# Optimization experiments

Measured on AMD Instinct MI355X. Metric: run time of the kernel, lower is better.

## Reference

```python
import jax, jax.numpy as jnp
import numpy as np
import math

NUM_HEADS = 16
HEAVY_RATIO = 0.1
RECENT_RATIO = 0.1
ROPE_THETA = 10000.0


def setup_inputs() -> dict:
    key = jax.random.key(0)
    ks = jax.random.split(key, 5)
    b, s, h = 1, 2048, 2048
    return {
        "hidden_states": jax.random.normal(ks[0], (b, s, h), dtype=jnp.float32),
        "Wq": jax.random.normal(ks[1], (h, h), dtype=jnp.float32) * 0.02,
        "Wk": jax.random.normal(ks[2], (h, h), dtype=jnp.float32) * 0.02,
        "Wv": jax.random.normal(ks[3], (h, h), dtype=jnp.float32) * 0.02,
        "Wo": jax.random.normal(ks[4], (h, h), dtype=jnp.float32) * 0.02,
    }


def _rotate_half(x):
    d = x.shape[-1]
    return jnp.concatenate([-x[..., d // 2:], x[..., : d // 2]], axis=-1)


def _rope(q, k, seq_len, head_dim, dtype):
    # LLaMA rotary embedding: inv_freq over even dims, emb = [freqs, freqs]
    inv_freq = 1.0 / (ROPE_THETA ** (jnp.arange(0, head_dim, 2, dtype=jnp.float32) / head_dim))
    pos = jnp.arange(seq_len, dtype=jnp.float32)
    freqs = pos[:, None] * inv_freq[None, :]            # [s, d/2]
    emb = jnp.concatenate([freqs, freqs], axis=-1)       # [s, d]
    cos = jnp.cos(emb).astype(dtype)[None, None]         # [1,1,s,d]
    sin = jnp.sin(emb).astype(dtype)[None, None]
    q = q * cos + _rotate_half(q) * sin
    k = k * cos + _rotate_half(k) * sin
    return q, k


def reference(hidden_states, Wq, Wk, Wv, Wo):
    b, s, hidden = hidden_states.shape
    H = NUM_HEADS
    d = hidden // H

    def proj(W):  # nn.Linear(x) = x @ W.T, then split heads -> [b,H,s,d]
        return (hidden_states @ W.T).reshape(b, s, H, d).transpose(0, 2, 1, 3)

    q, k, v = proj(Wq), proj(Wk), proj(Wv)
    q, k = _rope(q, k, s, d, hidden_states.dtype)

    scores = jnp.einsum("bhqd,bhkd->bhqk", q, k) / math.sqrt(d)  # [b,H,s,s]
    neg = jnp.finfo(scores.dtype).min
    i = jnp.arange(s)[:, None]
    j = jnp.arange(s)[None, :]
    causal = jnp.where(j <= i, jnp.array(0.0, scores.dtype), neg)
    scores = jnp.maximum(scores + causal, neg)

    heavy_budget = int(HEAVY_RATIO * s)
    recent_budget = int(RECENT_RATIO * s)

    # first softmax (fp32), accumulate column importances
    tmp_attn = jax.nn.softmax(scores.astype(jnp.float32), axis=-1).astype(scores.dtype)
    tmp_sum = jnp.sum(tmp_attn, axis=-2)                 # [b,H,s]
    _, topk_idx = jax.lax.top_k(tmp_sum, heavy_budget)   # [b,H,heavy]
    heavy_mask = jnp.any(topk_idx[..., :, None] == jnp.arange(s)[None, None, None, :], axis=-2)  # [b,H,s]

    # recent band: tril(diag=recent) & triu(diag=-recent)  <=>  |i-j| <= recent
    band = jnp.abs(i - j) <= recent_budget               # [s,s]
    mask = heavy_mask[:, :, None, :] | band[None, None]

    scores = jnp.where(mask, scores, neg)
    probs = jax.nn.softmax(scores.astype(jnp.float32), axis=-1).astype(q.dtype)
    attn = jnp.einsum("bhqk,bhkd->bhqd", probs, v)
    attn = attn.transpose(0, 2, 1, 3).reshape(b, s, hidden)
    return attn @ Wo.T
```

## Files before the change

kernel.cpp:

```cpp
#include <hip/hip_runtime.h>
#include <hip/hip_bf16.h>
#include <stdint.h>

#define SEQ   2048
#define HIDN  2048
#define NHEAD 16
#define HDIM  128
#define HEAVY 204
#define RECENT 204

typedef __attribute__((ext_vector_type(4))) float f32x4;
typedef __attribute__((ext_vector_type(8))) short bf16x8;
typedef unsigned short u16;
typedef unsigned int   u32;

static __device__ __forceinline__ u16 f2bf(float f){
  union { float f; u32 u; } v; v.f = f;
  u32 r = (v.u + 0x7FFFu + ((v.u >> 16) & 1u)) >> 16;
  return (u16)r;
}
static __device__ __forceinline__ float bf2f(u16 u){
  union { u32 u; float f; } v; v.u = ((u32)u) << 16;
  return v.f;
}

static __device__ __forceinline__ void gload16(const void* g, void* l){
  __builtin_amdgcn_global_load_lds((const __attribute__((address_space(1))) u32*)g,
                                   (__attribute__((address_space(3))) u32*)l, 16, 0, 0);
}

#define WAITVM(N) asm volatile("s_waitcnt vmcnt(" #N ")" ::: "memory")
#define BARRAW    __builtin_amdgcn_s_barrier()
#define PRIO1     __builtin_amdgcn_s_setprio(1)
#define PRIO0     __builtin_amdgcn_s_setprio(0)

static __device__ __forceinline__ void stage_tile(const u16* __restrict__ base, size_t stride,
                                                  int row0, u16* __restrict__ lds, int tid){
  const int wbase = tid & ~63;
#pragma unroll
  for (int it = 0; it < 4; ++it){
    int m = it * 256 + tid;
    int row = m >> 4, cp = m & 15;
    gload16(base + (size_t)(row0 + row) * stride + ((cp ^ (row & 7)) * 8),
            lds + (it * 256 + wbase) * 8);
  }
}

static __device__ __forceinline__ void stageK512(const u16* __restrict__ base, size_t stride,
                                                 int row0, u16* __restrict__ lds, int tid){
#pragma unroll
  for (int it = 0; it < 2; ++it){
    int m = it * 512 + tid;
    int row = m >> 4, cp = m & 15;
    gload16(base + (size_t)(row0 + row) * stride + ((cp ^ (row & 7)) * 8),
            lds + (it * 512 + (tid & ~63)) * 8);
  }
}
static __device__ __forceinline__ void stageV512(const u16* __restrict__ base, size_t stride,
                                                 int c0, u16* __restrict__ lds, int tid){
#pragma unroll
  for (int it = 0; it < 2; ++it){
    int m = it * 512 + tid;
    int row = m >> 3, cp = m & 7;
    gload16(base + (size_t)row * stride + c0 + ((cp ^ (row & 7)) * 8),
            lds + (it * 512 + (tid & ~63)) * 8);
  }
}

__global__ void k_prep(const float* __restrict__ A0, const float* __restrict__ A1,
                       const float* __restrict__ A2, const float* __restrict__ A3,
                       const float* __restrict__ A4, u16* __restrict__ out,
                       float* __restrict__ cosT, float* __restrict__ sinT,
                       float* __restrict__ colsum){
  int b = blockIdx.x, tid = threadIdx.x;
  if (b < 20480){
    int id = b * 256 + tid;
    int sel = id >> 20, off = (id & 1048575) * 4;
    const float* src = sel == 0 ? A0 : sel == 1 ? A1 : sel == 2 ? A2 : sel == 3 ? A3 : A4;
    float4 v = *(const float4*)(src + off);
    ushort4 o;
    o.x = f2bf(v.x); o.y = f2bf(v.y); o.z = f2bf(v.z); o.w = f2bf(v.w);
    *(ushort4*)(out + (size_t)sel * 4194304 + off) = o;
  } else if (b < 20992){
    int i = (b - 20480) * 256 + tid;
    int pos = i >> 6, j = i & 63;
    float invf = powf(10000.0f, -(float)j * (1.0f / 64.0f));
    float a = (float)pos * invf;
    cosT[i] = cosf(a);
    sinT[i] = sinf(a);
  } else {
    int i = (b - 20992) * 256 + tid;
    if (i < 16384) ((float4*)colsum)[i] = (float4){0.f, 0.f, 0.f, 0.f};
  }
}

__global__ void k_post(u16* __restrict__ Qm, u16* __restrict__ Km,
                       const float* __restrict__ cosT, const float* __restrict__ sinT,
                       const u16* __restrict__ V, u16* __restrict__ Vt){
  __shared__ u16 t[32][33];
  int b = blockIdx.x, tid = threadIdx.x;
  if (b < 4096){
    int gid = b * 256 + tid;
    u16* M = (gid < 524288) ? Qm : Km;
    int id = gid & 524287;
    int pos = id >> 8, rem = id & 255;
    int h = rem >> 4, j4 = (rem & 15) * 4;
    u16* p = M + (size_t)pos * HIDN + h * HDIM + j4;
    ushort4 lo = *(ushort4*)p;
    ushort4 hi = *(ushort4*)(p + 64);
    float4 c = *(const float4*)(cosT + pos * 64 + j4);
    float4 s = *(const float4*)(sinT + pos * 64 + j4);
    float l0 = bf2f(lo.x), l1 = bf2f(lo.y), l2 = bf2f(lo.z), l3 = bf2f(lo.w);
    float h0 = bf2f(hi.x), h1 = bf2f(hi.y), h2 = bf2f(hi.z), h3 = bf2f(hi.w);
    ushort4 nlo, nhi;
    nlo.x = f2bf(l0 * c.x - h0 * s.x);  nhi.x = f2bf(h0 * c.x + l0 * s.x);
    nlo.y = f2bf(l1 * c.y - h1 * s.y);  nhi.y = f2bf(h1 * c.y + l1 * s.y);
    nlo.z = f2bf(l2 * c.z - h2 * s.z);  nhi.z = f2bf(h2 * c.z + l2 * s.z);
    nlo.w = f2bf(l3 * c.w - h3 * s.w);  nhi.w = f2bf(h3 * c.w + l3 * s.w);
    *(ushort4*)p = nlo;
    *(ushort4*)(p + 64) = nhi;
  } else {
    int b2 = b - 4096;
    int s0 = (b2 & 63) * 32, c0 = (b2 >> 6) * 32;
    int r = tid >> 3, cc = (tid & 7) * 4;
    ushort4 v = *(const ushort4*)(V + (size_t)(s0 + r) * 2048 + c0 + cc);
    t[r][cc] = v.x; t[r][cc + 1] = v.y; t[r][cc + 2] = v.z; t[r][cc + 3] = v.w;
    __syncthreads();
    int co = tid >> 3, ro = (tid & 7) * 4;
    ushort4 o;
    o.x = t[ro][co]; o.y = t[ro + 1][co]; o.z = t[ro + 2][co]; o.w = t[ro + 3][co];
    *(ushort4*)(Vt + (size_t)(c0 + co) * 2048 + s0 + ro) = o;
  }
}

__global__ __launch_bounds__(512, 1)
void k_g256(const u16* __restrict__ X, const u16* __restrict__ Wq, const u16* __restrict__ Wk,
            const u16* __restrict__ Wv, u16* __restrict__ C0, u16* __restrict__ C1,
            u16* __restrict__ C2){
  __shared__ __align__(16) u16 LA[2][256 * 64];
  __shared__ __align__(16) u16 LB[2][192 * 64];
  const int tid = threadIdx.x;
  const int lane = tid & 63, wvi = tid >> 6;
  const int wm = wvi >> 2, wn = wvi & 3;
  const int g = lane >> 4, c15 = lane & 15;
  const int brow = blockIdx.y * 256;
  const int bcol = blockIdx.x * 192;
  const int NT = 32;

  f32x4 acc[8][3];
#pragma unroll
  for (int m = 0; m < 8; m++)
#pragma unroll
    for (int n = 0; n < 3; n++) acc[m][n] = (f32x4){0.f, 0.f, 0.f, 0.f};

  const int cc0 = ((g ^ (c15 & 7)) * 8);
  bf16x8 af[4][2], bf[3][2];

#define BPTR(rB_) (rB_ < 2048 ? Wq + (size_t)(rB_) * 2048 \
                 : rB_ < 4096 ? Wk + (size_t)((rB_) - 2048) * 2048 \
                              : Wv + (size_t)((rB_) - 4096) * 2048)
#define STGA(grow0, gcol0, ldsb) do { \
  _Pragma("unroll") for (int it = 0; it < 2; ++it){ \
    int m_ = it * 512 + tid; \
    int row_ = m_ >> 3, cp_ = m_ & 7; \
    gload16(X + (size_t)((grow0) + row_) * 2048 + (gcol0) + ((cp_ ^ (row_ & 7)) * 8), \
            (ldsb) + (it * 512 + (tid & ~63)) * 8); \
  } } while(0)
#define STGB128(gcol0, ldsb) do { \
  _Pragma("unroll") for (int it = 0; it < 2; ++it){ \
    int m_ = it * 512 + tid; \
    int row_ = m_ >> 3, cp_ = m_ & 7; \
    int rB_ = bcol + row_; \
    const u16* bp_ = BPTR(rB_); \
    gload16(bp_ + (gcol0) + ((cp_ ^ (row_ & 7)) * 8), \
            (ldsb) + (it * 512 + (tid & ~63)) * 8); \
  } } while(0)
#define STGB64(gcol0, ldsb) do { \
    int row_ = 128 + (tid >> 3), cp_ = tid & 7; \
    int rB_ = bcol + row_; \
    const u16* bp_ = BPTR(rB_); \
    gload16(bp_ + (gcol0) + ((cp_ ^ (row_ & 7)) * 8), \
            (ldsb) + (tid & ~63) * 8); \
  } while(0)
#define RDA(buf, mibase) \
  _Pragma("unroll") for (int mi2 = 0; mi2 < 4; ++mi2){ \
    const u16* pr = &LA[buf][0] + (size_t)(wm * 128 + ((mibase) + mi2) * 16 + c15) * 64; \
    af[mi2][0] = *(const bf16x8*)(pr + cc0); \
    af[mi2][1] = *(const bf16x8*)(pr + (cc0 ^ 32)); \
  }
#define RDB2(buf) \
  _Pragma("unroll") for (int ni2 = 0; ni2 < 2; ++ni2){ \
    const u16* pr = &LB[buf][0] + (size_t)(wn * 48 + ni2 * 16 + c15) * 64; \
    bf[ni2][0] = *(const bf16x8*)(pr + cc0); \
    bf[ni2][1] = *(const bf16x8*)(pr + (cc0 ^ 32)); \
  }
#define RDB1(buf) do { \
    const u16* pr = &LB[buf][0] + (size_t)(wn * 48 + 32 + c15) * 64; \
    bf[2][0] = *(const bf16x8*)(pr + cc0); \
    bf[2][1] = *(const bf16x8*)(pr + (cc0 ^ 32)); \
  } while(0)
#define MM2(mibase) \
  _Pragma("unroll") for (int mi2 = 0; mi2 < 4; ++mi2) \
  _Pragma("unroll") for (int ni2 = 0; ni2 < 2; ++ni2) \
  _Pragma("unroll") for (int kk = 0; kk < 2; ++kk) \
    acc[(mibase) + mi2][ni2] = __builtin_amdgcn_mfma_f32_16x16x32_bf16( \
        af[mi2][kk], bf[ni2][kk], acc[(mibase) + mi2][ni2], 0, 0, 0);
#define MM1(mibase) \
  _Pragma("unroll") for (int mi2 = 0; mi2 < 4; ++mi2) \
  _Pragma("unroll") for (int kk = 0; kk < 2; ++kk) \
    acc[(mibase) + mi2][2] = __builtin_amdgcn_mfma_f32_16x16x32_bf16( \
        af[mi2][kk], bf[2][kk], acc[(mibase) + mi2][2], 0, 0, 0);

  STGA(brow,       0, &LA[0][0]);
  STGA(brow + 128, 0, &LA[0][0] + 128 * 64);
  STGB128(0,  &LB[0][0]);
  STGB64(0,   &LB[0][0] + 128 * 64);
  STGB128(64, &LB[1][0]);
  STGB64(64,  &LB[1][0] + 128 * 64);
  WAITVM(3);
  BARRAW;

  for (int t = 0; t < NT; t += 2){
    const int kn1 = (t + 1) * 64;
    const int kn2 = (t + 2) * 64;
    const int kn3 = (t + 3) * 64;
    RDA(0, 0); RDB2(0);
    STGA(brow, kn1, &LA[1][0]);
    BARRAW; PRIO1; MM2(0); PRIO0; BARRAW;
    RDB1(0);
    STGA(brow + 128, kn1, &LA[1][0] + 128 * 64);
    BARRAW; PRIO1; MM1(0); PRIO0; BARRAW;
    RDA(0, 4);
    if (t + 2 < NT) STGB128(kn2, &LB[0][0]);
    BARRAW; PRIO1; MM1(4); PRIO0; BARRAW;
    if (t + 2 < NT){ STGB64(kn2, &LB[0][0] + 128 * 64); WAITVM(3); }
    else            { WAITVM(0); }
    BARRAW; PRIO1; MM2(4); PRIO0; BARRAW;
    RDA(1, 0); RDB2(1);
    if (t + 2 < NT) STGA(brow, kn2, &LA[0][0]);
    BARRAW; PRIO1; MM2(0); PRIO0; BARRAW;
    RDB1(1);
    if (t + 2 < NT) STGA(brow + 128, kn2, &LA[0][0] + 128 * 64);
    BARRAW; PRIO1; MM1(0); PRIO0; BARRAW;
    RDA(1, 4);
    if (t + 3 < NT) STGB128(kn3, &LB[1][0]);
    BARRAW; PRIO1; MM1(4); PRIO0; BARRAW;
    if (t + 3 < NT){ STGB64(kn3, &LB[1][0] + 128 * 64); WAITVM(3); }
    else if (t + 2 < NT){ WAITVM(0); }
    BARRAW; PRIO1; MM2(4); PRIO0; BARRAW;
  }
#undef BPTR
#undef STGA
#undef STGB128
#undef STGB64
#undef RDA
#undef RDB2
#undef RDB1
#undef MM2
#undef MM1

#pragma unroll
  for (int mi = 0; mi < 8; ++mi)
#pragma unroll
    for (int ni = 0; ni < 3; ++ni){
      int colbase = bcol + wn * 48 + ni * 16;
      int proj = colbase >> 11;
      u16* Cb = proj == 0 ? C0 : proj == 1 ? C1 : C2;
      int lc = (colbase & 2047) + c15;
#pragma unroll
      for (int r = 0; r < 4; ++r){
        int row = brow + wm * 128 + mi * 16 + g * 4 + r;
        Cb[(size_t)row * 2048 + lc] = f2bf(acc[mi][ni][r]);
      }
    }
}

__global__ __launch_bounds__(512)
void k_gemm_out(const u16* __restrict__ A, const u16* __restrict__ B, float* __restrict__ C){
  __shared__ __align__(16) u16 As[2][128 * 64];
  __shared__ __align__(16) u16 Bs[2][128 * 64];
  const int tid = threadIdx.x;
  const int w = tid >> 6, lane = tid & 63;
  const int wm = w >> 1, wn = w & 1;
  const int g = lane >> 4, c15 = lane & 15;
  const int brow = blockIdx.y * 128, bcol = blockIdx.x * 128;
  const int cc0 = ((g ^ (c15 & 7)) * 8);

  f32x4 acc[2][4];
#pragma unroll
  for (int m = 0; m < 2; m++)
#pragma unroll
    for (int n = 0; n < 4; n++) acc[m][n] = (f32x4){0.f, 0.f, 0.f, 0.f};

#define STG_O(k0, buf) do { \
  _Pragma("unroll") for (int it = 0; it < 2; ++it){ \
    int m_ = it * 512 + tid; \
    int row_ = m_ >> 3, cp_ = m_ & 7; \
    gload16(A + (size_t)(brow + row_) * 2048 + (k0) + ((cp_ ^ (row_ & 7)) * 8), \
            As[buf] + (it * 512 + (tid & ~63)) * 8); \
    gload16(B + (size_t)(bcol + row_) * 2048 + (k0) + ((cp_ ^ (row_ & 7)) * 8), \
            Bs[buf] + (it * 512 + (tid & ~63)) * 8); \
  } } while(0)

  STG_O(0, 0);
  int cur = 0;
  for (int kt = 0; kt < 32; ++kt){
    if (kt + 1 < 32){ STG_O((kt + 1) * 64, cur ^ 1); WAITVM(4); }
    else            { WAITVM(0); }
    BARRAW;
    bf16x8 af[2][2], bfr[4][2];
#pragma unroll
    for (int mi = 0; mi < 2; ++mi){
      const u16* pr = As[cur] + (size_t)(wm * 32 + mi * 16 + c15) * 64;
      af[mi][0] = *(const bf16x8*)(pr + cc0);
      af[mi][1] = *(const bf16x8*)(pr + (cc0 ^ 32));
    }
#pragma unroll
    for (int ni = 0; ni < 4; ++ni){
      const u16* pr = Bs[cur] + (size_t)(wn * 64 + ni * 16 + c15) * 64;
      bfr[ni][0] = *(const bf16x8*)(pr + cc0);
      bfr[ni][1] = *(const bf16x8*)(pr + (cc0 ^ 32));
    }
    PRIO1;
#pragma unroll
    for (int mi = 0; mi < 2; ++mi)
#pragma unroll
      for (int ni = 0; ni < 4; ++ni)
#pragma unroll
        for (int kk = 0; kk < 2; ++kk)
          acc[mi][ni] = __builtin_amdgcn_mfma_f32_16x16x32_bf16(af[mi][kk], bfr[ni][kk],
                                                                acc[mi][ni], 0, 0, 0);
    PRIO0;
    BARRAW;
    cur ^= 1;
  }
#undef STG_O
#pragma unroll
  for (int mi = 0; mi < 2; ++mi)
#pragma unroll
    for (int ni = 0; ni < 4; ++ni)
#pragma unroll
      for (int r = 0; r < 4; ++r){
        int row = brow + wm * 32 + mi * 16 + g * 4 + r;
        int col = bcol + wn * 64 + ni * 16 + c15;
        C[(size_t)row * 2048 + col] = acc[mi][ni][r];
      }
}

__global__ __launch_bounds__(256)
void k_pass1a(const u16* __restrict__ Q, const u16* __restrict__ K, float* __restrict__ rowsum){
  __shared__ __align__(16) u16 Ks[2][64 * 128];
  const int tid = threadIdx.x;
  const int wv = tid >> 6, lane = tid & 63;
  const int g = lane >> 4, c15 = lane & 15;
  const int h = blockIdx.y;
  int qb = 0, c = 0;
  { int rem = blockIdx.x; int q = 0;
    while (rem >= ((2 * q + 9) >> 3)){ rem -= (2 * q + 9) >> 3; q++; }
    qb = q; c = rem; }
  const int i0 = qb * 128;
  const int ktend = 2 * qb + 2;
  const int kt0 = c * 8;
  const int kt1 = (ktend < kt0 + 8) ? ktend : (kt0 + 8);
  const u16* Qh = Q + h * HDIM;
  const u16* Kh = K + h * HDIM;
  const float scale = 0.08838834764831845f;
  const int wb = wv * 32;

  bf16x8 qfr[2][4];
#pragma unroll
  for (int m = 0; m < 2; m++)
#pragma unroll
    for (int ks = 0; ks < 4; ks++)
      qfr[m][ks] = *(const bf16x8*)(Qh + (size_t)(i0 + wb + m * 16 + c15) * 2048 + ks * 32 + g * 8);

  stage_tile(Kh, 2048, kt0 * 64, Ks[0], tid);

  float rs[2][4] = {{0.f,0.f,0.f,0.f},{0.f,0.f,0.f,0.f}};
  int cur = 0;
  for (int kt = kt0; kt < kt1; ++kt){
    if (kt + 1 < kt1){ stage_tile(Kh, 2048, (kt + 1) * 64, Ks[cur ^ 1], tid); WAITVM(4); }
    else             { WAITVM(0); }
    BARRAW;
    const int k0 = kt * 64;
    f32x4 sacc[2][4];
#pragma unroll
    for (int m = 0; m < 2; m++)
#pragma unroll
      for (int n = 0; n < 4; n++) sacc[m][n] = (f32x4){0.f, 0.f, 0.f, 0.f};
#pragma unroll
    for (int ks = 0; ks < 4; ++ks){
#pragma unroll
      for (int n = 0; n < 4; n++){
        int brw = n * 16 + c15;
        bf16x8 b = *(const bf16x8*)(Ks[cur] + brw * 128 + ((ks * 32 + g * 8) ^ ((brw & 7) << 3)));
#pragma unroll
        for (int m = 0; m < 2; m++)
          sacc[m][n] = __builtin_amdgcn_mfma_f32_16x16x32_bf16(qfr[m][ks], b, sacc[m][n], 0, 0, 0);
      }
    }
    if (kt < 2 * qb){
#pragma unroll
      for (int m = 0; m < 2; m++)
#pragma unroll
        for (int n = 0; n < 4; n++)
#pragma unroll
          for (int r = 0; r < 4; r++)
            rs[m][r] += __expf(sacc[m][n][r] * scale);
    } else {
#pragma unroll
      for (int n = 0; n < 4; n++){
        int col = k0 + n * 16 + c15;
#pragma unroll
        for (int m = 0; m < 2; m++)
#pragma unroll
          for (int r = 0; r < 4; r++){
            int rowg = i0 + wb + m * 16 + g * 4 + r;
            rs[m][r] += (col <= rowg) ? __expf(sacc[m][n][r] * scale) : 0.f;
          }
      }
    }
    BARRAW;
    cur ^= 1;
  }
#pragma unroll
  for (int m = 0; m < 2; m++)
#pragma unroll
    for (int r = 0; r < 4; r++){
      float v = rs[m][r];
      v += __shfl_xor(v, 1); v += __shfl_xor(v, 2);
      v += __shfl_xor(v, 4); v += __shfl_xor(v, 8);
      if (c15 == 0)
        atomicAdd(&rowsum[h * 2048 + i0 + wb + m * 16 + g * 4 + r], v);
    }
}

__global__ __launch_bounds__(256)
void k_pass1b(const u16* __restrict__ Q, const u16* __restrict__ K,
              const float* __restrict__ rowsum, float* __restrict__ colsum){
  __shared__ __align__(16) u16 Qs[2][64 * 128];
  const int tid = threadIdx.x;
  const int wv = tid >> 6, lane = tid & 63;
  const int g = lane >> 4, c15 = lane & 15;
  const int h = blockIdx.y;
  int kb = 0, c = 0;
  { int rem = blockIdx.x; int q = 0;
    while (rem >= ((39 - 2 * q) >> 3)){ rem -= (39 - 2 * q) >> 3; q++; }
    kb = q; c = rem; }
  const int k0 = kb * 128;
  const int qt0 = 2 * kb + c * 8;
  const int qt1 = (2 * kb + c * 8 + 8 < 32) ? (2 * kb + c * 8 + 8) : 32;
  const u16* Qh = Q + h * HDIM;
  const u16* Kh = K + h * HDIM;
  const float scale = 0.08838834764831845f;
  const int wb = wv * 32;
  const float* rsrow = rowsum + h * 2048;

  bf16x8 kfr[2][4];
#pragma unroll
  for (int m = 0; m < 2; m++)
#pragma unroll
    for (int ks = 0; ks < 4; ks++)
      kfr[m][ks] = *(const bf16x8*)(Kh + (size_t)(k0 + wb + m * 16 + c15) * 2048 + ks * 32 + g * 8);

  stage_tile(Qh, 2048, qt0 * 64, Qs[0], tid);

  float racc[2][4] = {{0.f,0.f,0.f,0.f},{0.f,0.f,0.f,0.f}};
  int cur = 0;
  for (int qt = qt0; qt < qt1; ++qt){
    if (qt + 1 < qt1){ stage_tile(Qh, 2048, (qt + 1) * 64, Qs[cur ^ 1], tid); WAITVM(4); }
    else             { WAITVM(0); }
    BARRAW;
    const int i0q = qt * 64;
    float rw[4];
#pragma unroll
    for (int n = 0; n < 4; n++)
      rw[n] = 1.0f / rsrow[i0q + n * 16 + c15];
    f32x4 sacc[2][4];
#pragma unroll
    for (int m = 0; m < 2; m++)
#pragma unroll
      for (int n = 0; n < 4; n++) sacc[m][n] = (f32x4){0.f, 0.f, 0.f, 0.f};
#pragma unroll
    for (int ks = 0; ks < 4; ++ks){
#pragma unroll
      for (int n = 0; n < 4; n++){
        int brw = n * 16 + c15;
        bf16x8 b = *(const bf16x8*)(Qs[cur] + brw * 128 + ((ks * 32 + g * 8) ^ ((brw & 7) << 3)));
#pragma unroll
        for (int m = 0; m < 2; m++)
          sacc[m][n] = __builtin_amdgcn_mfma_f32_16x16x32_bf16(kfr[m][ks], b, sacc[m][n], 0, 0, 0);
      }
    }
    if (qt >= 2 * kb + 2){
#pragma unroll
      for (int m = 0; m < 2; m++)
#pragma unroll
        for (int n = 0; n < 4; n++)
#pragma unroll
          for (int r = 0; r < 4; r++)
            racc[m][r] += __expf(sacc[m][n][r] * scale) * rw[n];
    } else {
#pragma unroll
      for (int n = 0; n < 4; n++){
        int colq = i0q + n * 16 + c15;
#pragma unroll
        for (int m = 0; m < 2; m++)
#pragma unroll
          for (int r = 0; r < 4; r++){
            int rowk = k0 + wb + m * 16 + g * 4 + r;
            racc[m][r] += (rowk <= colq) ? __expf(sacc[m][n][r] * scale) * rw[n] : 0.f;
          }
      }
    }
    BARRAW;
    cur ^= 1;
  }
#pragma unroll
  for (int m = 0; m < 2; m++)
#pragma unroll
    for (int r = 0; r < 4; r++){
      float v = racc[m][r];
      v += __shfl_xor(v, 1); v += __shfl_xor(v, 2);
      v += __shfl_xor(v, 4); v += __shfl_xor(v, 8);
      if (c15 == 0)
        atomicAdd(&colsum[h * 2048 + k0 + wb + m * 16 + g * 4 + r], v);
    }
}

__global__ __launch_bounds__(1024)
void k_topkg(const float* __restrict__ colsum, const u16* __restrict__ Kb,
             const u16* __restrict__ Vb, short* __restrict__ cidx,
             u16* __restrict__ Kg, u16* __restrict__ Vg){
  __shared__ u32 keys[2048];
  __shared__ int hist[256];
  __shared__ int chunkCnt[32];
  __shared__ short cidL[256];
  __shared__ u32 Tacc_s;
  __shared__ int rem_s;
  __shared__ __align__(16) u16 t[32][136];
  const int tid = threadIdx.x;
  const int h = blockIdx.x;
  const int w = tid >> 6, lane = tid & 63;

  for (int i = tid; i < 2048; i += 1024) keys[i] = ((const u32*)colsum)[h * 2048 + i];
  if (tid == 0){ Tacc_s = 0; rem_s = HEAVY; }
  __syncthreads();

  for (int s = 24; s >= 0; s -= 8){
    if (tid < 256) hist[tid] = 0;
    __syncthreads();
    u32 T = Tacc_s;
    for (int i = tid; i < 2048; i += 1024){
      u32 k = keys[i];
      bool match = (s == 24) ? true : (((k ^ T) >> (s + 8)) == 0);
      if (match) atomicAdd(&hist[(k >> s) & 255], 1);
    }
    __syncthreads();
    if (tid == 0){
      int rem = rem_s, acc = 0, b = 255;
      for (; b > 0; --b){
        int c2 = hist[b];
        if (acc + c2 >= rem) break;
        acc += c2;
      }
      Tacc_s = T | ((u32)b << s);
      rem_s = rem - acc;
    }
    __syncthreads();
  }
  const u32 T = Tacc_s;
  const int need = rem_s;
  const u32 kA = keys[tid], kB = keys[tid + 1024];
  const bool eqA = (kA == T), eqB = (kB == T);
  unsigned long long ebA = __ballot(eqA);
  unsigned long long ebB = __ballot(eqB);
  if (lane == 0){ chunkCnt[w] = __popcll(ebA); chunkCnt[16 + w] = __popcll(ebB); }
  __syncthreads();
  if (tid == 0){
    int s2 = 0;
    for (int i2 = 0; i2 < 32; ++i2){ int c2 = chunkCnt[i2]; chunkCnt[i2] = s2; s2 += c2; }
  }
  __syncthreads();
  const unsigned long long below = (1ull << lane) - 1ull;
  const int eqrA = chunkCnt[w] + __popcll(ebA & below);
  const int eqrB = chunkCnt[16 + w] + __popcll(ebB & below);
  const bool hvA = (kA > T) || (eqA && eqrA < need);
  const bool hvB = (kB > T) || (eqB && eqrB < need);
  __syncthreads();
  unsigned long long hbA = __ballot(hvA);
  unsigned long long hbB = __ballot(hvB);
  if (lane == 0){ chunkCnt[w] = __popcll(hbA); chunkCnt[16 + w] = __popcll(hbB); }
  if (tid >= HEAVY && tid < 256) cidL[tid] = 32767;
  __syncthreads();
  if (tid == 0){
    int s2 = 0;
    for (int i2 = 0; i2 < 32; ++i2){ int c2 = chunkCnt[i2]; chunkCnt[i2] = s2; s2 += c2; }
  }
  __syncthreads();
  if (hvA) cidL[chunkCnt[w] + __popcll(hbA & below)] = (short)tid;
  if (hvB) cidL[chunkCnt[16 + w] + __popcll(hbB & below)] = (short)(tid + 1024);
  __syncthreads();
  if (tid < 256) cidx[h * 256 + tid] = cidL[tid];

  for (int i = tid; i < 4096; i += 1024){
    int slot = i >> 4, cp = i & 15;
    int cid = cidL[slot];
    bf16x8 z = (bf16x8){0,0,0,0,0,0,0,0};
    bf16x8 val = (cid < 2048) ? *(const bf16x8*)(Kb + (size_t)cid * 2048 + h * 128 + cp * 8) : z;
    *(bf16x8*)(Kg + ((size_t)h * 256 + slot) * 128 + cp * 8) = val;
  }
  for (int grp = 0; grp < 8; ++grp){
    int s0 = grp * 32;
    if (tid < 512){
      int s2 = tid >> 4, cp = tid & 15;
      int cid = cidL[s0 + s2];
      bf16x8 z = (bf16x8){0,0,0,0,0,0,0,0};
      bf16x8 val = (cid < 2048) ? *(const bf16x8*)(Vb + (size_t)cid * 2048 + h * 128 + cp * 8) : z;
      *(bf16x8*)(&t[s2][cp * 8]) = val;
    }
    __syncthreads();
    for (int i = tid; i < 4096; i += 1024){
      int d = i >> 5, s2 = i & 31;
      Vg[((size_t)h * 128 + d) * 256 + s0 + s2] = t[s2][d];
    }
    __syncthreads();
  }
}

__global__ __launch_bounds__(512)
void k_pass2(const u16* __restrict__ Q, const u16* __restrict__ K, const u16* __restrict__ Vt,
             const u16* __restrict__ Kg, const u16* __restrict__ Vg,
             const short* __restrict__ cidx, u16* __restrict__ attn){
  __shared__ __align__(16) u16 Ks[2][64 * 128];
  __shared__ __align__(16) u16 Vs[2][128 * 64];
  __shared__ __align__(16) u16 Ps[8][16 * 64];
  __shared__ short cids[256];
  __shared__ int lists[12];
  __shared__ int nact_s;
  const int tid = threadIdx.x;
  const int w = tid >> 6, lane = tid & 63;
  const int g = lane >> 4, c15 = lane & 15;
  const int qb = blockIdx.x, h = blockIdx.y;
  const int i0 = qb * 128;
  const int wq = w >> 2, w4 = w & 3;
  const int rowbase = i0 + wq * 64 + w4 * 16;
  const u16* Qh = Q + h * HDIM;
  const u16* Kh = K + h * HDIM;
  const u16* Kgh = Kg + (size_t)h * 256 * 128;
  const u16* Vth = Vt + (size_t)h * 128 * 2048;
  const u16* Vgh = Vg + (size_t)h * 128 * 256;
  const float scale = 0.08838834764831845f;

  if (tid < 256) cids[tid] = cidx[h * 256 + tid];
  bf16x8 qfr[4];
#pragma unroll
  for (int ks = 0; ks < 4; ks++)
    qfr[ks] = *(const bf16x8*)(Qh + (size_t)(rowbase + c15) * 2048 + ks * 32 + g * 8);
  __syncthreads();
  if (tid == 0){
    int n = 0;
    int ktb0 = (i0 > RECENT) ? ((i0 - RECENT) >> 6) : 0;
    int ktmax = (i0 + 127) >> 6;
    for (int kt = ktb0; kt <= ktmax; ++kt) lists[n++] = kt;
    for (int gt = 0; gt < 4; ++gt)
      if ((int)cids[gt * 64] <= i0 + 127 - RECENT - 1) lists[n++] = 100 + gt;
    nact_s = n;
  }
  __syncthreads();
  const int nact = nact_s;

  { int e = lists[0];
    if (e < 100){ stageK512(Kh, 2048, e * 64, Ks[0], tid);
                  stageV512(Vth, 2048, e * 64, Vs[0], tid); }
    else        { stageK512(Kgh, 128, (e - 100) * 64, Ks[0], tid);
                  stageV512(Vgh, 256, (e - 100) * 64, Vs[0], tid); } }
  WAITVM(2);
  BARRAW;

  f32x4 oacc[8];
#pragma unroll
  for (int f = 0; f < 8; f++) oacc[f] = (f32x4){0.f, 0.f, 0.f, 0.f};
  float lsum[4] = {0.f, 0.f, 0.f, 0.f};

  int cur = 0;
  for (int i = 0; i < nact; ++i){
    const int e = lists[i];
    const bool isg = (e >= 100);
    const bool nxt = (i + 1 < nact);
    if (nxt){
      int e2 = lists[i + 1];
      if (e2 < 100){ stageK512(Kh, 2048, e2 * 64, Ks[cur ^ 1], tid);
                     stageV512(Vth, 2048, e2 * 64, Vs[cur ^ 1], tid); }
      else         { stageK512(Kgh, 128, (e2 - 100) * 64, Ks[cur ^ 1], tid);
                     stageV512(Vgh, 256, (e2 - 100) * 64, Vs[cur ^ 1], tid); }
      WAITVM(6);
    } else {
      WAITVM(2);
    }
    BARRAW;
    f32x4 sacc[4];
#pragma unroll
    for (int n = 0; n < 4; n++) sacc[n] = (f32x4){0.f, 0.f, 0.f, 0.f};
#pragma unroll
    for (int ks = 0; ks < 4; ++ks){
#pragma unroll
      for (int n = 0; n < 4; n++){
        int brw = n * 16 + c15;
        bf16x8 b = *(const bf16x8*)(Ks[cur] + brw * 128 + ((ks * 32 + g * 8) ^ ((brw & 7) << 3)));
        sacc[n] = __builtin_amdgcn_mfma_f32_16x16x32_bf16(qfr[ks], b, sacc[n], 0, 0, 0);
      }
    }
#pragma unroll
    for (int n = 0; n < 4; n++){
      int cid = isg ? (int)cids[(e - 100) * 64 + n * 16 + c15] : (e * 64 + n * 16 + c15);
#pragma unroll
      for (int r = 0; r < 4; r++){
        int rowg = rowbase + g * 4 + r;
        int dist = rowg - cid;
        bool valid = (cid <= rowg) && (isg ? (dist > RECENT) : (dist <= RECENT));
        float ev = valid ? __expf(sacc[n][r] * scale) : 0.f;
        lsum[r] += ev;
        int prow = g * 4 + r;
        Ps[w][prow * 64 + ((n * 16 + c15) ^ ((prow & 7) << 3))] = f2bf(ev);
      }
    }
    if (nxt) WAITVM(4); else WAITVM(0);
    BARRAW;
    PRIO1;
#pragma unroll
    for (int ks2 = 0; ks2 < 2; ++ks2){
      bf16x8 pa = *(const bf16x8*)(&Ps[w][c15 * 64 + ((ks2 * 32 + g * 8) ^ ((c15 & 7) << 3))]);
#pragma unroll
      for (int f = 0; f < 8; ++f){
        int vrow = f * 16 + c15;
        bf16x8 vb = *(const bf16x8*)(Vs[cur] + vrow * 64 + ((ks2 * 32 + g * 8) ^ ((vrow & 7) << 3)));
        oacc[f] = __builtin_amdgcn_mfma_f32_16x16x32_bf16(pa, vb, oacc[f], 0, 0, 0);
      }
    }
    PRIO0;
    BARRAW;
    cur ^= 1;
  }
  float rinv[4];
#pragma unroll
  for (int r = 0; r < 4; r++){
    float v = lsum[r];
    v += __shfl_xor(v, 1); v += __shfl_xor(v, 2);
    v += __shfl_xor(v, 4); v += __shfl_xor(v, 8);
    rinv[r] = 1.0f / v;
  }
#pragma unroll
  for (int f = 0; f < 8; f++)
#pragma unroll
    for (int r = 0; r < 4; r++){
      int rowg = rowbase + g * 4 + r;
      attn[(size_t)rowg * 2048 + h * HDIM + f * 16 + c15] = f2bf(oacc[f][r] * rinv[r]);
    }
}

extern "C" void kernel_launch(void* const* d_in, const int* in_sizes, int n_in,
                              void* d_out, int out_size, void* d_ws, size_t ws_size,
                              hipStream_t stream){
  const float* X  = (const float*)d_in[0];
  const float* Wq = (const float*)d_in[1];
  const float* Wk = (const float*)d_in[2];
  const float* Wv = (const float*)d_in[3];
  const float* Wo = (const float*)d_in[4];

  char* w = (char*)d_ws;
  const size_t MB8 = (size_t)2048 * 2048 * 2;
  u16* Xb  = (u16*)(w);
  u16* Wqb = (u16*)(w + 1 * MB8);
  u16* Wkb = (u16*)(w + 2 * MB8);
  u16* Wvb = (u16*)(w + 3 * MB8);
  u16* Wob = (u16*)(w + 4 * MB8);
  u16* Qb  = (u16*)(w + 5 * MB8);
  u16* Kb  = (u16*)(w + 6 * MB8);
  u16* Vb  = (u16*)(w + 7 * MB8);
  u16* Vtb   = Wqb;
  u16* attnb = Xb;
  char* p = w + 8 * MB8;
  float* cosT = (float*)p;              p += 524288;
  float* sinT = (float*)p;              p += 524288;
  float* colsum = (float*)p;            p += 131072;
  float* rowsum = (float*)p;            p += 131072;
  short* cidx  = (short*)p;             p += 16 * 256 * 2;
  u16*   Kg    = (u16*)p;               p += (size_t)16 * 256 * 128 * 2;
  u16*   Vg    = (u16*)p;

  dim3 b256(256);

  k_prep<<<21056, b256, 0, stream>>>(X, Wq, Wk, Wv, Wo, Xb, cosT, sinT, colsum);

  k_g256<<<dim3(32, 8), dim3(512), 0, stream>>>(Xb, Wqb, Wkb, Wvb, Qb, Kb, Vb);
  k_post<<<8192, b256, 0, stream>>>(Qb, Kb, cosT, sinT, Vb, Vtb);

  k_pass1a<<<dim3(40, 16), b256, 0, stream>>>(Qb, Kb, rowsum);
  k_pass1b<<<dim3(40, 16), b256, 0, stream>>>(Qb, Kb, rowsum, colsum);
  k_topkg<<<16, dim3(1024), 0, stream>>>(colsum, Kb, Vb, cidx, Kg, Vg);
  k_pass2<<<dim3(16, 16), dim3(512), 0, stream>>>(Qb, Kb, Vtb, Kg, Vg, cidx, attnb);

  k_gemm_out<<<dim3(16, 16), dim3(512), 0, stream>>>(attnb, Wob, (float*)d_out);
}
```

Measured before the change: 246.9 us.

## Restructure QKV GEMM pipeline into 3-phase tiles and split top-k gather kernel

```diff
diff --git a/kernel.cpp b/kernel.cpp
--- a/kernel.cpp
+++ b/kernel.cpp
@@ -154,7 +154,7 @@
     for (int n = 0; n < 3; n++) acc[m][n] = (f32x4){0.f, 0.f, 0.f, 0.f};
 
   const int cc0 = ((g ^ (c15 & 7)) * 8);
-  bf16x8 af[4][2], bf[3][2];
+  bf16x8 af[4][2], af2[4][2], bf[3][2];
 
 #define BPTR(rB_) (rB_ < 2048 ? Wq + (size_t)(rB_) * 2048 \
                  : rB_ < 4096 ? Wk + (size_t)((rB_) - 2048) * 2048 \
@@ -182,11 +182,17 @@
     gload16(bp_ + (gcol0) + ((cp_ ^ (row_ & 7)) * 8), \
             (ldsb) + (tid & ~63) * 8); \
   } while(0)
-#define RDA(buf, mibase) \
+#define RDA(buf) \
   _Pragma("unroll") for (int mi2 = 0; mi2 < 4; ++mi2){ \
-    const u16* pr = &LA[buf][0] + (size_t)(wm * 128 + ((mibase) + mi2) * 16 + c15) * 64; \
+    const u16* pr = &LA[buf][0] + (size_t)(wm * 128 + mi2 * 16 + c15) * 64; \
     af[mi2][0] = *(const bf16x8*)(pr + cc0); \
     af[mi2][1] = *(const bf16x8*)(pr + (cc0 ^ 32)); \
+  }
+#define RDA2(buf) \
+  _Pragma("unroll") for (int mi2 = 0; mi2 < 4; ++mi2){ \
+    const u16* pr = &LA[buf][0] + (size_t)(wm * 128 + (4 + mi2) * 16 + c15) * 64; \
+    af2[mi2][0] = *(const bf16x8*)(pr + cc0); \
+    af2[mi2][1] = *(const bf16x8*)(pr + (cc0 ^ 32)); \
   }
 #define RDB2(buf) \
   _Pragma("unroll") for (int ni2 = 0; ni2 < 2; ++ni2){ \
@@ -199,17 +205,44 @@
     bf[2][0] = *(const bf16x8*)(pr + cc0); \
     bf[2][1] = *(const bf16x8*)(pr + (cc0 ^ 32)); \
   } while(0)
-#define MM2(mibase) \
+#define MM2A \
   _Pragma("unroll") for (int mi2 = 0; mi2 < 4; ++mi2) \
   _Pragma("unroll") for (int ni2 = 0; ni2 < 2; ++ni2) \
   _Pragma("unroll") for (int kk = 0; kk < 2; ++kk) \
-    acc[(mibase) + mi2][ni2] = __builtin_amdgcn_mfma_f32_16x16x32_bf16( \
-        af[mi2][kk], bf[ni2][kk], acc[(mibase) + mi2][ni2], 0, 0, 0);
-#define MM1(mibase) \
+    acc[mi2][ni2] = __builtin_amdgcn_mfma_f32_16x16x32_bf16( \
+        af[mi2][kk], bf[ni2][kk], acc[mi2][ni2], 0, 0, 0);
+#define MM1AB \
   _Pragma("unroll") for (int mi2 = 0; mi2 < 4; ++mi2) \
+  _Pragma("unroll") for (int kk = 0; kk < 2; ++kk){ \
+    acc[mi2][2] = __builtin_amdgcn_mfma_f32_16x16x32_bf16( \
+        af[mi2][kk], bf[2][kk], acc[mi2][2], 0, 0, 0); \
+    acc[4 + mi2][2] = __builtin_amdgcn_mfma_f32_16x16x32_bf16( \
+        af2[mi2][kk], bf[2][kk], acc[4 + mi2][2], 0, 0, 0); \
+  }
+#define MM2B \
+  _Pragma("unroll") for (int mi2 = 0; mi2 < 4; ++mi2) \
+  _Pragma("unroll") for (int ni2 = 0; ni2 < 2; ++ni2) \
   _Pragma("unroll") for (int kk = 0; kk < 2; ++kk) \
-    acc[(mibase) + mi2][2] = __builtin_amdgcn_mfma_f32_16x16x32_bf16( \
-        af[mi2][kk], bf[2][kk], acc[(mibase) + mi2][2], 0, 0, 0);
+    acc[4 + mi2][ni2] = __builtin_amdgcn_mfma_f32_16x16x32_bf16( \
+        af2[mi2][kk], bf[ni2][kk], acc[4 + mi2][ni2], 0, 0, 0);
+
+#define TILE(t, buf) do { \
+    const int kn1 = ((t) + 1) * 64; \
+    const int kn2 = ((t) + 2) * 64; \
+     \
+    RDA(buf); RDB2(buf); \
+    if ((t) + 1 < NT) STGA(brow, kn1, &LA[buf ^ 1][0]); \
+    BARRAW; PRIO1; MM2A; PRIO0; BARRAW; \
+     \
+    RDB1(buf); RDA2(buf); \
+    if ((t) + 1 < NT) STGA(brow + 128, kn1, &LA[buf ^ 1][0] + 128 * 64); \
+    BARRAW; PRIO1; MM1AB; PRIO0; BARRAW; \
+     \
+    if ((t) + 2 < NT){ STGB128(kn2, &LB[buf][0]); STGB64(kn2, &LB[buf][0] + 128 * 64); \
+                       WAITVM(3); } \
+    else             { WAITVM(0); } \
+    BARRAW; PRIO1; MM2B; PRIO0; BARRAW; \
+  } while(0)
 
   STGA(brow,       0, &LA[0][0]);
   STGA(brow + 128, 0, &LA[0][0] + 128 * 64);
@@ -221,43 +254,21 @@
   BARRAW;
 
   for (int t = 0; t < NT; t += 2){
-    const int kn1 = (t + 1) * 64;
-    const int kn2 = (t + 2) * 64;
-    const int kn3 = (t + 3) * 64;
-    RDA(0, 0); RDB2(0);
-    STGA(brow, kn1, &LA[1][0]);
-    BARRAW; PRIO1; MM2(0); PRIO0; BARRAW;
-    RDB1(0);
-    STGA(brow + 128, kn1, &LA[1][0] + 128 * 64);
-    BARRAW; PRIO1; MM1(0); PRIO0; BARRAW;
-    RDA(0, 4);
-    if (t + 2 < NT) STGB128(kn2, &LB[0][0]);
-    BARRAW; PRIO1; MM1(4); PRIO0; BARRAW;
-    if (t + 2 < NT){ STGB64(kn2, &LB[0][0] + 128 * 64); WAITVM(3); }
-    else            { WAITVM(0); }
-    BARRAW; PRIO1; MM2(4); PRIO0; BARRAW;
-    RDA(1, 0); RDB2(1);
-    if (t + 2 < NT) STGA(brow, kn2, &LA[0][0]);
-    BARRAW; PRIO1; MM2(0); PRIO0; BARRAW;
-    RDB1(1);
-    if (t + 2 < NT) STGA(brow + 128, kn2, &LA[0][0] + 128 * 64);
-    BARRAW; PRIO1; MM1(0); PRIO0; BARRAW;
-    RDA(1, 4);
-    if (t + 3 < NT) STGB128(kn3, &LB[1][0]);
-    BARRAW; PRIO1; MM1(4); PRIO0; BARRAW;
-    if (t + 3 < NT){ STGB64(kn3, &LB[1][0] + 128 * 64); WAITVM(3); }
-    else if (t + 2 < NT){ WAITVM(0); }
-    BARRAW; PRIO1; MM2(4); PRIO0; BARRAW;
-  }
+    TILE(t, 0);
+    TILE(t + 1, 1);
+  }
+#undef TILE
 #undef BPTR
 #undef STGA
 #undef STGB128
 #undef STGB64
 #undef RDA
+#undef RDA2
 #undef RDB2
 #undef RDB1
-#undef MM2
-#undef MM1
+#undef MM2A
+#undef MM1AB
+#undef MM2B
 
 #pragma unroll
   for (int mi = 0; mi < 8; ++mi)
@@ -529,16 +540,13 @@
 }
 
 __global__ __launch_bounds__(1024)
-void k_topkg(const float* __restrict__ colsum, const u16* __restrict__ Kb,
-             const u16* __restrict__ Vb, short* __restrict__ cidx,
-             u16* __restrict__ Kg, u16* __restrict__ Vg){
+void k_topk(const float* __restrict__ colsum, short* __restrict__ cidx){
   __shared__ u32 keys[2048];
   __shared__ int hist[256];
   __shared__ int chunkCnt[32];
   __shared__ short cidL[256];
   __shared__ u32 Tacc_s;
   __shared__ int rem_s;
-  __shared__ __align__(16) u16 t[32][136];
   const int tid = threadIdx.x;
   const int h = blockIdx.x;
   const int w = tid >> 6, lane = tid & 63;
@@ -602,29 +610,40 @@
   if (hvB) cidL[chunkCnt[16 + w] + __popcll(hbB & below)] = (short)(tid + 1024);
   __syncthreads();
   if (tid < 256) cidx[h * 256 + tid] = cidL[tid];
-
-  for (int i = tid; i < 4096; i += 1024){
-    int slot = i >> 4, cp = i & 15;
-    int cid = cidL[slot];
+}
+
+__global__ void k_gath(const u16* __restrict__ Kb, const u16* __restrict__ Vb,
+                       const short* __restrict__ cidx,
+                       u16* __restrict__ Kg, u16* __restrict__ Vg){
+  __shared__ __align__(16) u16 t[32][136];
+  int b = blockIdx.x, tid = threadIdx.x;
+  if (b < 256){
+    int gid = b * 256 + tid;
+    int h = gid >> 12, rem = gid & 4095;
+    int slot = rem >> 4, cp = rem & 15;
+    int cid = cidx[h * 256 + slot];
     bf16x8 z = (bf16x8){0,0,0,0,0,0,0,0};
     bf16x8 val = (cid < 2048) ? *(const bf16x8*)(Kb + (size_t)cid * 2048 + h * 128 + cp * 8) : z;
     *(bf16x8*)(Kg + ((size_t)h * 256 + slot) * 128 + cp * 8) = val;
-  }
-  for (int grp = 0; grp < 8; ++grp){
-    int s0 = grp * 32;
-    if (tid < 512){
-      int s2 = tid >> 4, cp = tid & 15;
-      int cid = cidL[s0 + s2];
+  } else {
+    int b2 = b - 256;
+    int h = b2 >> 3, s0 = (b2 & 7) * 32;
+#pragma unroll
+    for (int it = 0; it < 2; ++it){
+      int m = it * 256 + tid;
+      int s = m >> 4, cp = m & 15;
+      int cid = cidx[h * 256 + s0 + s];
       bf16x8 z = (bf16x8){0,0,0,0,0,0,0,0};
       bf16x8 val = (cid < 2048) ? *(const bf16x8*)(Vb + (size_t)cid * 2048 + h * 128 + cp * 8) : z;
-      *(bf16x8*)(&t[s2][cp * 8]) = val;
+      *(bf16x8*)(&t[s][cp * 8]) = val;
     }
     __syncthreads();
-    for (int i = tid; i < 4096; i += 1024){
-      int d = i >> 5, s2 = i & 31;
-      Vg[((size_t)h * 128 + d) * 256 + s0 + s2] = t[s2][d];
-    }
-    __syncthreads();
+#pragma unroll
+    for (int i = 0; i < 16; ++i){
+      int idx = i * 256 + tid;
+      int d = idx >> 5, s = idx & 31;
+      Vg[((size_t)h * 128 + d) * 256 + s0 + s] = t[s][d];
+    }
   }
 }
 
@@ -798,7 +817,8 @@
 
   k_pass1a<<<dim3(40, 16), b256, 0, stream>>>(Qb, Kb, rowsum);
   k_pass1b<<<dim3(40, 16), b256, 0, stream>>>(Qb, Kb, rowsum, colsum);
-  k_topkg<<<16, dim3(1024), 0, stream>>>(colsum, Kb, Vb, cidx, Kg, Vg);
+  k_topk<<<16, dim3(1024), 0, stream>>>(colsum, cidx);
+  k_gath<<<384, b256, 0, stream>>>(Kb, Vb, cidx, Kg, Vg);
   k_pass2<<<dim3(16, 16), dim3(512), 0, stream>>>(Qb, Kb, Vtb, Kg, Vg, cidx, attnb);
 
   k_gemm_out<<<dim3(16, 16), dim3(512), 0, stream>>>(attnb, Wob, (float*)d_out);
```

Measured after the change: 243.0 us. No clear change (-1.6%).
